# Optimization experiments

Measured on AMD Instinct MI355X. Metric: run time of the kernel, lower is better.

The kernel has to match this reference:

```python
import jax, jax.numpy as jnp
import numpy as np

B, L, D_MODEL = 2, 1024, 512
N_LAYERS = 4
D_INNER = 2 * D_MODEL          # expand=2
D_STATE = 16
D_CONV = 4
DT_RANK = D_MODEL // 16        # ceil(512/16)=32
EPS = 1e-5


def layernorm(x, w, b):
    m = jnp.mean(x, axis=-1, keepdims=True)
    v = jnp.var(x, axis=-1, keepdims=True)
    return (x - m) * jax.lax.rsqrt(v + EPS) * w + b


def selective_scan(u, delta, A, Bm, Cm, Dp):
    # u, delta: [b,l,d]; Bm, Cm: [b,l,n]; A: [d,n]; Dp: [d]
    def step(h, inp):
        dt_t, b_t, c_t, u_t = inp            # [b,d],[b,n],[b,n],[b,d]
        dA = jnp.exp(dt_t[:, :, None] * A)   # [b,d,n]
        h = dA * h + (dt_t * u_t)[:, :, None] * b_t[:, None, :]
        y = jnp.einsum('bdn,bn->bd', h, c_t)
        return h, y

    b, l, d = u.shape
    n = A.shape[1]
    h0 = jnp.zeros((b, d, n), u.dtype)
    xs = (jnp.swapaxes(delta, 0, 1), jnp.swapaxes(Bm, 0, 1),
          jnp.swapaxes(Cm, 0, 1), jnp.swapaxes(u, 0, 1))
    _, ys = jax.lax.scan(step, h0, xs)       # ys: [l,b,d]
    return jnp.swapaxes(ys, 0, 1) + u * Dp


def mamba(x, in_w, conv_w, conv_b, xp_w, dtp_w, dtp_b, A_log, Dp, out_w):
    # x: [b,l,D_MODEL]
    xz = x @ in_w.T                          # [b,l,2*d_inner]
    xc, z = jnp.split(xz, 2, axis=-1)
    xc = jnp.swapaxes(xc, 1, 2)              # [b,d_inner,l]
    xc = jax.lax.conv_general_dilated(
        xc, conv_w[:, None, :], (1,), [(D_CONV - 1, 0)],
        feature_group_count=D_INNER,
        dimension_numbers=('NCH', 'OIH', 'NCH')) + conv_b[None, :, None]
    xc = jax.nn.silu(jnp.swapaxes(xc, 1, 2))  # [b,l,d_inner]
    x_dbl = xc @ xp_w.T                       # [b,l,dt_rank+2n]
    dt = x_dbl[..., :DT_RANK]
    Bm = x_dbl[..., DT_RANK:DT_RANK + D_STATE]
    Cm = x_dbl[..., DT_RANK + D_STATE:]
    dt = jax.nn.softplus(dt @ dtp_w.T + dtp_b)
    A = -jnp.exp(A_log)
    y = selective_scan(xc, dt, A, Bm, Cm, Dp)
    y = y * jax.nn.silu(z)
    return y @ out_w.T


def forward(x, in_proj_w, conv_w, conv_b, x_proj_w, dt_proj_w, dt_proj_b,
            A_log, D_param, out_proj_w, ln_w, ln_b, fnorm_w, fnorm_b):
    residual = None
    for i in range(in_proj_w.shape[0]):
        residual = x if residual is None else x + residual
        xn = layernorm(x, ln_w[i], ln_b[i])  # norm of incoming x (as in torch src)
        h1 = mamba(xn, in_proj_w[i, 0], conv_w[i, 0], conv_b[i, 0],
                   x_proj_w[i, 0], dt_proj_w[i, 0], dt_proj_b[i, 0],
                   A_log[i, 0], D_param[i, 0], out_proj_w[i, 0])
        h2 = mamba(jnp.flip(xn, axis=1), in_proj_w[i, 1], conv_w[i, 1],
                   conv_b[i, 1], x_proj_w[i, 1], dt_proj_w[i, 1],
                   dt_proj_b[i, 1], A_log[i, 1], D_param[i, 1],
                   out_proj_w[i, 1])
        x = h1 + h2                           # bi_add: NOT flipped back, faithful
    x = x + residual
    return layernorm(x, fnorm_w, fnorm_b)


def setup_inputs() -> dict:
    key = jax.random.key(0)
    ks = jax.random.split(key, 8)
    P2 = (N_LAYERS, 2)
    inp = {}
    inp['x'] = jax.random.normal(ks[0], (B, L, D_MODEL), jnp.float32)
    inp['in_proj_w'] = jax.random.normal(ks[1], P2 + (2 * D_INNER, D_MODEL), jnp.float32) * 0.02
    inp['conv_w'] = jax.random.normal(ks[2], P2 + (D_INNER, D_CONV), jnp.float32) * 0.1
    inp['conv_b'] = jnp.zeros(P2 + (D_INNER,), jnp.float32)
    inp['x_proj_w'] = jax.random.normal(ks[3], P2 + (DT_RANK + 2 * D_STATE, D_INNER), jnp.float32) * 0.02
    inp['dt_proj_w'] = jax.random.normal(ks[4], P2 + (D_INNER, DT_RANK), jnp.float32) * (DT_RANK ** -0.5)
    inp['dt_proj_b'] = jnp.full(P2 + (D_INNER,), float(np.log(np.expm1(0.01))), jnp.float32)
    inp['A_log'] = jnp.broadcast_to(jnp.log(jnp.arange(1, D_STATE + 1, dtype=jnp.float32)), P2 + (D_INNER, D_STATE)).copy()
    inp['D_param'] = jnp.ones(P2 + (D_INNER,), jnp.float32)
    inp['out_proj_w'] = jax.random.normal(ks[5], P2 + (D_MODEL, D_INNER), jnp.float32) * 0.02
    inp['ln_w'] = jnp.ones((N_LAYERS, D_MODEL), jnp.float32)
    inp['ln_b'] = jnp.zeros((N_LAYERS, D_MODEL), jnp.float32)
    inp['fnorm_w'] = jnp.ones((D_MODEL,), jnp.float32)
    inp['fnorm_b'] = jnp.zeros((D_MODEL,), jnp.float32)
    return inp


def reference(x, in_proj_w, conv_w, conv_b, x_proj_w, dt_proj_w, dt_proj_b,
              A_log, D_param, out_proj_w, ln_w, ln_b, fnorm_w, fnorm_b):
    return forward(x, in_proj_w, conv_w, conv_b, x_proj_w, dt_proj_w,
                   dt_proj_b, A_log, D_param, out_proj_w, ln_w, ln_b,
                   fnorm_w, fnorm_b)
```

## Files before the change

kernel.cpp:

```cpp
#include <hip/hip_runtime.h>
#include <hip/hip_bf16.h>
#include <type_traits>

#define B_   2
#define L_   1024
#define DM   512
#define DI   1024
#define DS   16
#define DTR  32
#define ROWS (B_*L_)
#define NCH  32
#define CHUNK (L_/NCH)

#define PO_CW    0
#define PO_CB    32768
#define PO_XPW   40960
#define PO_DTW   565248
#define PO_DTB   827392
#define PO_ALOG  835584
#define PO_DP    966656
#define PO_LNW   974848
#define PO_LNB   976896
#define PO_FNW   978944
#define PO_FNB   979456
#define PO_END   979968

#define N_WIN    (4*2097152)
#define N_WOUT   (4*1048576)
#define N_X      1048576

typedef __bf16 bf16x8 __attribute__((ext_vector_type(8)));
typedef float  f32x4  __attribute__((ext_vector_type(4)));
using bf16 = __hip_bfloat16;

__device__ __forceinline__ bf16x8 ld8(const bf16* p){
    return *reinterpret_cast<const bf16x8*>(p);
}
__device__ __forceinline__ float b2f(bf16 v){ return __bfloat162float(v); }

__device__ __forceinline__ unsigned pkbf2(float a, float b){
    bf16 ha = __float2bfloat16(a), hb = __float2bfloat16(b);
    unsigned short ua = *(unsigned short*)&ha, ub = *(unsigned short*)&hb;
    return (unsigned)ua | ((unsigned)ub << 16);
}
__device__ __forceinline__ float unpk_lo(unsigned v){
    unsigned x = v << 16; return __builtin_bit_cast(float, x);
}
__device__ __forceinline__ float unpk_hi(unsigned v){
    unsigned x = v & 0xffff0000u; return __builtin_bit_cast(float, x);
}

__device__ __forceinline__ void async_cp16(const void* g, void* s){
    __builtin_amdgcn_global_load_lds(
        (const __attribute__((address_space(1))) unsigned int*)g,
        (__attribute__((address_space(3))) unsigned int*)s, 16, 0, 0);
}

__global__ void detect_kernel(const void* Dp_raw, int* flag){
    *flag = (*(const unsigned int*)Dp_raw == 0x3F800000u) ? 1 : 0;
}

__device__ __forceinline__ bf16 cvload(const void* s, long o, int f){
    return f ? __float2bfloat16(((const float*)s)[o]) : ((const bf16*)s)[o];
}

__global__ void megacvt_kernel(const void* cw, const void* cb, const void* xpw,
                               const void* dtw, const void* dtb, const void* al,
                               const void* dp, const void* lnw, const void* lnb,
                               const void* fnw, const void* fnb,
                               const void* inw, const void* outw, const void* xin,
                               bf16* PP, bf16* WIN, bf16* WOUT,
                               float* X, float* R, const int* flag){
    long i = (long)blockIdx.x*256 + threadIdx.x;
    int f = *flag;
    if (i < PO_END){
        const void* s; long o;
        if      (i < PO_CB)   { s = cw;  o = i; }
        else if (i < PO_XPW)  { s = cb;  o = i - PO_CB; }
        else if (i < PO_DTW)  { s = xpw; o = i - PO_XPW; }
        else if (i < PO_DTB)  { s = dtw; o = i - PO_DTW; }
        else if (i < PO_ALOG) { s = dtb; o = i - PO_DTB; }
        else if (i < PO_DP)   { s = al;  o = i - PO_ALOG; }
        else if (i < PO_LNW)  { s = dp;  o = i - PO_DP; }
        else if (i < PO_LNB)  { s = lnw; o = i - PO_LNW; }
        else if (i < PO_FNW)  { s = lnb; o = i - PO_LNB; }
        else if (i < PO_FNB)  { s = fnw; o = i - PO_FNW; }
        else                  { s = fnb; o = i - PO_FNB; }
        PP[i] = cvload(s, o, f);
        return;
    }
    i -= PO_END;
    if (i < N_WIN){ WIN[i] = cvload(inw, i, f); return; }
    i -= N_WIN;
    if (i < N_WOUT){
        long l = i >> 20, r = i & 1048575;
        long n = r >> 11, dir = (r >> 10) & 1, d = r & 1023;
        WOUT[i] = cvload(outw, ((l*2 + dir)*512 + n)*1024 + d, f);
        return;
    }
    i -= N_WOUT;
    if (i < N_X){
        X[i] = f ? ((const float*)xin)[i] : b2f(((const bf16*)xin)[i]);
        R[i] = 0.f;
    }
}

__global__ void ln_kernel(const float* __restrict__ P, int nparts,
                          float* __restrict__ R,
                          const bf16* __restrict__ w, const bf16* __restrict__ b,
                          void* __restrict__ out, int mode, const int* flag){
    int row = blockIdx.x, lane = threadIdx.x;
    size_t base = (size_t)row*DM + lane*8;
    float v[8];
    *(float4*)&v[0] = *(const float4*)(P+base);
    *(float4*)&v[4] = *(const float4*)(P+base+4);
    for (int k=1; k<nparts; ++k){
        float4 a0 = *(const float4*)(P + (size_t)k*1048576 + base);
        float4 a1 = *(const float4*)(P + (size_t)k*1048576 + base + 4);
        v[0]+=a0.x; v[1]+=a0.y; v[2]+=a0.z; v[3]+=a0.w;
        v[4]+=a1.x; v[5]+=a1.y; v[6]+=a1.z; v[7]+=a1.w;
    }
    if (mode == 0){
        float4 r0 = *(const float4*)(R+base);
        float4 r1 = *(const float4*)(R+base+4);
        r0.x += v[0]; r0.y += v[1]; r0.z += v[2]; r0.w += v[3];
        r1.x += v[4]; r1.y += v[5]; r1.z += v[6]; r1.w += v[7];
        *(float4*)(R+base)   = r0;
        *(float4*)(R+base+4) = r1;
    } else {
        float4 r0 = *(const float4*)(R+base);
        float4 r1 = *(const float4*)(R+base+4);
        v[0]+=r0.x; v[1]+=r0.y; v[2]+=r0.z; v[3]+=r0.w;
        v[4]+=r1.x; v[5]+=r1.y; v[6]+=r1.z; v[7]+=r1.w;
    }
    float s=0.f, sq=0.f;
    #pragma unroll
    for (int j=0;j<8;++j){ s += v[j]; sq += v[j]*v[j]; }
    #pragma unroll
    for (int off=32; off>=1; off>>=1){
        s  += __shfl_xor(s,  off, 64);
        sq += __shfl_xor(sq, off, 64);
    }
    float mean = s*(1.f/DM);
    float var  = sq*(1.f/DM) - mean*mean;
    float rs   = rsqrtf(var + 1e-5f);
    bf16x8 wv = ld8(w + lane*8), bv = ld8(b + lane*8);
    float res[8];
    #pragma unroll
    for (int j=0;j<8;++j)
        res[j] = (v[j]-mean)*rs*(float)wv[j] + (float)bv[j];
    if (mode == 1 && *flag){
        float* of = (float*)out;
        *(float4*)(of+base)   = make_float4(res[0],res[1],res[2],res[3]);
        *(float4*)(of+base+4) = make_float4(res[4],res[5],res[6],res[7]);
    } else {
        union { bf16 h[8]; uint4 u; } o;
        #pragma unroll
        for (int j=0;j<8;++j) o.h[j] = __float2bfloat16(res[j]);
        *(uint4*)((bf16*)out + base) = o.u;
    }
}

template<int WM, int WN, int SK, int BK, typename CT>
__global__ __launch_bounds__(WM*WN*64)
void gemm_lds(const bf16* __restrict__ A, const bf16* __restrict__ W,
              CT* __restrict__ C, int K, int lda, int ldw, int ldc,
              int selTiles, long wSel){
    constexpr int BM = WM*64, BN = WN*64, T = WM*WN*64;
    constexpr int KC = BK/8;
    constexpr int RA = (BM*KC)/T, RB = (BN*KC)/T;
    __shared__ __align__(16) bf16 sA[BM*BK];
    __shared__ __align__(16) bf16 sB[BN*BK];
    int tid = threadIdx.x;
    int mtile = blockIdx.y, ntile = blockIdx.x;
    if (mtile >= selTiles) W += wSel;
    int m0 = mtile*BM, n0 = ntile*BN;
    int kPer = K/SK, kBeg = blockIdx.z*kPer, kEnd = kBeg + kPer;
    if (SK > 1)
        C += (size_t)blockIdx.z * (size_t)(gridDim.y*BM) * (size_t)(gridDim.x*BN);
    int wave = tid>>6, lane = tid&63, quad = lane>>4, r = lane&15;
    int wrow = wave / WN, wcol = wave % WN;
    const bf16* Abase = A + (size_t)m0*lda;
    const bf16* Wbase = W + (size_t)n0*ldw;
    f32x4 acc[4][4] = {};
    for (int k0 = kBeg; k0 < kEnd; k0 += BK){
        #pragma unroll
        for (int rr=0; rr<RA; ++rr){
            int q = rr*T + tid;
            int row = q/KC, cp = q%KC;
            async_cp16(Abase + (size_t)row*lda + k0 + cp*8, &sA[q*8]);
        }
        #pragma unroll
        for (int rr=0; rr<RB; ++rr){
            int q = rr*T + tid;
            int row = q/KC, cp = q%KC;
            async_cp16(Wbase + (size_t)row*ldw + k0 + cp*8, &sB[q*8]);
        }
        __syncthreads();
        #pragma unroll
        for (int ko=0; ko<BK; ko+=32){
            bf16x8 af[4], bw[4];
            #pragma unroll
            for (int mt=0; mt<4; ++mt)
                af[mt] = *(const bf16x8*)&sA[(wrow*64 + mt*16 + r)*BK + ko + quad*8];
            #pragma unroll
            for (int nt=0; nt<4; ++nt)
                bw[nt] = *(const bf16x8*)&sB[(wcol*64 + nt*16 + r)*BK + ko + quad*8];
            #pragma unroll
            for (int mt=0; mt<4; ++mt)
                #pragma unroll
                for (int nt=0; nt<4; ++nt)
                    acc[mt][nt] = __builtin_amdgcn_mfma_f32_16x16x32_bf16(
                        af[mt], bw[nt], acc[mt][nt], 0,0,0);
        }
        __syncthreads();
    }
    #pragma unroll
    for (int mt=0; mt<4; ++mt){
        #pragma unroll
        for (int nt=0; nt<4; ++nt){
            int col = n0 + wcol*64 + nt*16 + r;
            #pragma unroll
            for (int ri=0; ri<4; ++ri){
                int row = m0 + wrow*64 + mt*16 + quad*4 + ri;
                size_t idx = (size_t)row*ldc + col;
                if constexpr (std::is_same<CT, bf16>::value)
                    C[idx] = __float2bfloat16(acc[mt][nt][ri]);
                else
                    C[idx] = acc[mt][nt][ri];
            }
        }
    }
}

__global__ void conv_kernel(const bf16* __restrict__ XZ, const bf16* __restrict__ cw,
                            const bf16* __restrict__ cb, const bf16* __restrict__ Dp,
                            bf16* __restrict__ XC, unsigned* __restrict__ GU){
    int id  = blockIdx.x*256 + threadIdx.x;
    int d   = (id & 511) * 2;
    int t   = (id >> 9) & (L_-1);
    int b   = (id >> 19) & 1;
    int dir = id >> 20;
    bf16x8 wv8 = ld8(cw + ((size_t)dir*DI + d)*4);
    unsigned pcb = *(const unsigned*)&cb[dir*DI + d];
    float acc0 = unpk_lo(pcb), acc1 = unpk_hi(pcb);
    #pragma unroll
    for (int k=0;k<4;++k){
        int tau = t - 3 + k;
        if (tau >= 0){
            int sig = dir ? (L_-1-tau) : tau;
            unsigned pz = *(const unsigned*)&XZ[((size_t)(b*L_ + sig))*4096 + dir*2048 + d];
            acc0 += (float)wv8[k]   * unpk_lo(pz);
            acc1 += (float)wv8[4+k] * unpk_hi(pz);
        }
    }
    float u0 = acc0 * (1.f/(1.f + __expf(-acc0)));
    float u1 = acc1 * (1.f/(1.f + __expf(-acc1)));
    size_t idx = ((size_t)dir*ROWS + (size_t)b*L_ + t)*DI + d;
    *(unsigned*)&XC[idx] = pkbf2(u0, u1);
    int sig3 = dir ? (L_-1-t) : t;
    unsigned pzz = *(const unsigned*)&XZ[((size_t)(b*L_ + sig3))*4096 + dir*2048 + 1024 + d];
    float z0 = unpk_lo(pzz), z1 = unpk_hi(pzz);
    float g0 = z0*(1.f/(1.f + __expf(-z0)));
    float g1 = z1*(1.f/(1.f + __expf(-z1)));
    unsigned pdv = *(const unsigned*)&Dp[dir*DI + d];
    *(uint2*)&GU[idx] = make_uint2(pkbf2(g0, u0*unpk_lo(pdv)*g0),
                                   pkbf2(g1, u1*unpk_hi(pdv)*g1));
}

__global__ void dtproj_kernel(const float* __restrict__ PX, const bf16* __restrict__ dtw,
                              const bf16* __restrict__ dtb, const bf16* __restrict__ XC,
                              unsigned* __restrict__ DTW, float* __restrict__ XD){
    int id  = blockIdx.x*256 + threadIdx.x;
    int d   = id & (DI-1);
    int row = (id >> 10) & (ROWS-1);
    int dir = id >> 21;
    int tid = threadIdx.x;
    int grow = dir*2048 + row;
    __shared__ float sXR[32];
    if (tid < 32){
        float s = 0.f;
        #pragma unroll
        for (int k=0;k<8;++k) s += PX[(size_t)k*262144 + (size_t)grow*64 + tid];
        sXR[tid] = s;
    } else if (tid < 64 && ((id >> 8) & 3) == 0){
        int j = tid - 32;
        float s = 0.f;
        #pragma unroll
        for (int k=0;k<8;++k) s += PX[(size_t)k*262144 + (size_t)grow*64 + 32 + j];
        XD[(size_t)row*128 + dir*64 + 32 + j] = s;
    }
    __syncthreads();
    const bf16* wp = dtw + ((size_t)dir*DI + d)*DTR;
    float acc = b2f(dtb[dir*DI + d]);
    #pragma unroll
    for (int kk=0;kk<4;++kk){
        bf16x8 wv = ld8(wp + kk*8);
        #pragma unroll
        for (int j=0;j<8;++j) acc += sXR[kk*8+j]*(float)wv[j];
    }
    float sp = acc > 20.f ? acc : log1pf(__expf(acc));
    size_t idx = ((size_t)dir*ROWS + row)*DI + d;
    float u = b2f(XC[idx]);
    DTW[idx] = pkbf2(sp, sp*u);
}

template<int PHASE>
__global__ __launch_bounds__(256)
void scan_phase(const unsigned* __restrict__ DTW, const unsigned* __restrict__ GU,
                const float* __restrict__ XD, const bf16* __restrict__ Al,
                float* __restrict__ SP, float* __restrict__ SH,
                bf16* __restrict__ Y){
    int dirb = blockIdx.z, dir = dirb >> 1, b = dirb & 1;
    int c    = blockIdx.y;
    int d0   = blockIdx.x*128;
    int tid  = threadIdx.x;
    int dl   = tid >> 1, nh = tid & 1;
    int d    = d0 + dl;

    __shared__ __align__(16) unsigned sDTW[CHUNK*128];
    __shared__ __align__(16) float    sBC[CHUNK][32];
    __shared__ __align__(16) unsigned sGU[(PHASE==3)?CHUNK*128:4];

    const unsigned* DTWb = DTW + ((size_t)dir*ROWS + b*L_ + c*CHUNK)*DI + d0;
    #pragma unroll
    for (int it=0; it<4; ++it){
        int q = it*256 + tid;
        int t = q >> 5, c4 = q & 31;
        async_cp16(DTWb + (size_t)t*DI + c4*4, &sDTW[q*4]);
    }
    if (PHASE == 3){
        const unsigned* GUb = GU + ((size_t)dir*ROWS + b*L_ + c*CHUNK)*DI + d0;
        #pragma unroll
        for (int it=0; it<4; ++it){
            int q = it*256 + tid;
            int t = q >> 5, c4 = q & 31;
            async_cp16(GUb + (size_t)t*DI + c4*4, &sGU[q*4]);
        }
    }
    {
        int t = tid >> 3, j = tid & 7;
        async_cp16(XD + ((size_t)(b*L_) + c*CHUNK + t)*128 + dir*64 + 32 + j*4,
                   &sBC[t][j*4]);
    }

    float An[8];
    {
        const bf16* ap = Al + ((size_t)dir*DI + d)*DS + nh*8;
        bf16x8 av = ld8(ap);
        #pragma unroll
        for (int j=0;j<8;++j) An[j] = -__expf((float)av[j]);
    }

    float h[8], pr[8];
    #pragma unroll
    for (int j=0;j<8;++j){ h[j]=0.f; pr[j]=1.f; }
    size_t so = ((size_t)(dirb*NCH + c)*DI + d)*DS + nh*8;
    if (PHASE == 3){
        for (int cc=0; cc<c; ++cc){
            size_t o = ((size_t)(dirb*NCH + cc)*DI + d)*DS + nh*8;
            f32x4 p0 = *(const f32x4*)&SP[o];
            f32x4 p1 = *(const f32x4*)&SP[o+4];
            f32x4 h0 = *(const f32x4*)&SH[o];
            f32x4 h1 = *(const f32x4*)&SH[o+4];
            #pragma unroll
            for (int j=0;j<4;++j){
                h[j]   = p0[j]*h[j]   + h0[j];
                h[4+j] = p1[j]*h[4+j] + h1[j];
            }
        }
    }
    __syncthreads();

    bf16* Yp = Y + ((size_t)b*L_ + c*CHUNK)*2048 + dir*DI + d;

    #pragma unroll 4
    for (int tl=0; tl<CHUNK; ++tl){
        unsigned dw = sDTW[tl*128 + dl];
        float dtv = unpk_lo(dw), wv = unpk_hi(dw);
        f32x4 Bv0 = *(const f32x4*)&sBC[tl][nh*8];
        f32x4 Bv1 = *(const f32x4*)&sBC[tl][nh*8+4];
        f32x4 Cv0 = *(const f32x4*)&sBC[tl][16+nh*8];
        f32x4 Cv1 = *(const f32x4*)&sBC[tl][16+nh*8+4];
        float y = 0.f;
        #pragma unroll
        for (int j=0;j<4;++j){
            float dA0 = __expf(dtv*An[j]);
            float dA1 = __expf(dtv*An[4+j]);
            h[j]   = dA0*h[j]   + wv*Bv0[j];
            h[4+j] = dA1*h[4+j] + wv*Bv1[j];
            if (PHASE == 1){ pr[j] *= dA0; pr[4+j] *= dA1; }
            else { y += h[j]*Cv0[j]; y += h[4+j]*Cv1[j]; }
        }
        if (PHASE == 3){
            y += __shfl_xor(y, 1, 64);
            if (nh == 0){
                unsigned gu = sGU[tl*128 + dl];
                Yp[(size_t)tl*2048] = __float2bfloat16(y*unpk_lo(gu) + unpk_hi(gu));
            }
        }
    }
    if (PHASE == 1){
        *(f32x4*)&SP[so]   = *(f32x4*)&pr[0];
        *(f32x4*)&SP[so+4] = *(f32x4*)&pr[4];
        *(f32x4*)&SH[so]   = *(f32x4*)&h[0];
        *(f32x4*)&SH[so+4] = *(f32x4*)&h[4];
    }
}

extern "C" void kernel_launch(void* const* d_in, const int* in_sizes, int n_in,
                              void* d_out, int out_size, void* d_ws, size_t ws_size,
                              hipStream_t stream){
    const void* x_raw    = d_in[0];
    const void* inw_raw  = d_in[1];
    const void* convw_raw= d_in[2];
    const void* convb_raw= d_in[3];
    const void* xpw_raw  = d_in[4];
    const void* dtw_raw  = d_in[5];
    const void* dtb_raw  = d_in[6];
    const void* alog_raw = d_in[7];
    const void* dp_raw   = d_in[8];
    const void* outw_raw = d_in[9];
    const void* lnw_raw  = d_in[10];
    const void* lnb_raw  = d_in[11];
    const void* fnw_raw  = d_in[12];
    const void* fnb_raw  = d_in[13];

    char* ws = (char*)d_ws;
    float*    X   = (float*)   (ws + 0);
    float*    R   = (float*)   (ws + 4194304);
    bf16*     XN  = (bf16*)    (ws + 8388608);
    bf16*     XZ  = (bf16*)    (ws + 10485760);
    bf16*     XC  = (bf16*)    (ws + 27262976);
    float*    XD  = (float*)   (ws + 35651584);
    unsigned* DTW = (unsigned*)(ws + 36700160);
    unsigned* GU  = (unsigned*)(ws + 52428800);
    bf16*     Y   = (bf16*)    (ws + 68157440);
    float*    SP  = (float*)   (ws + 76546048);
    float*    SH  = (float*)   (ws + 84934656);
    bf16*     PP  = (bf16*)    (ws + 93323264);
    bf16*     WIN = (bf16*)    (ws + 95420416);
    bf16*     WOUT= (bf16*)    (ws + 112197632);
    float*    PX  = (float*)   (ws + 120586240);
    float*    PO  = (float*)   (ws + 128974848);
    int*      FLAG= (int*)     (ws + 145752064);

    detect_kernel<<<1,1,0,stream>>>(dp_raw, FLAG);
    {
        long total = (long)PO_END + N_WIN + N_WOUT + N_X;
        int blocks = (int)((total + 255)/256);
        megacvt_kernel<<<blocks,256,0,stream>>>(
            convw_raw, convb_raw, xpw_raw, dtw_raw, dtb_raw, alog_raw, dp_raw,
            lnw_raw, lnb_raw, fnw_raw, fnb_raw, inw_raw, outw_raw, x_raw,
            PP, WIN, WOUT, X, R, FLAG);
    }

    for (int l=0; l<4; ++l){
        ln_kernel<<<ROWS,64,0,stream>>>(l==0 ? X : PO, l==0 ? 1 : 4, R,
                                        PP+PO_LNW+l*DM, PP+PO_LNB+l*DM, XN, 0, FLAG);

        gemm_lds<2,2,1,64,bf16><<<dim3(32,16,1),256,0,stream>>>(
            XN, WIN + (size_t)l*2097152, XZ, 512, 512, 512, 4096, 1<<30, 0);

        conv_kernel<<<8192,256,0,stream>>>(XZ, PP+PO_CW + (size_t)l*2*DI*4,
                                           PP+PO_CB + l*2*DI, PP+PO_DP + l*2*DI,
                                           XC, GU);

        gemm_lds<2,1,8,64,float><<<dim3(1,32,8),128,0,stream>>>(
            XC, PP+PO_XPW + (size_t)l*2*64*DI, PX, 1024, 1024, 1024, 64,
            16, (long)64*DI);

        dtproj_kernel<<<16384,256,0,stream>>>(PX, PP+PO_DTW + (size_t)l*2*DI*DTR,
                                              PP+PO_DTB + l*2*DI, XC, DTW, XD);

        scan_phase<1><<<dim3(DI/128,NCH,4),256,0,stream>>>(
            DTW, GU, XD, PP+PO_ALOG + (size_t)l*2*DI*DS, SP, SH, Y);
        scan_phase<3><<<dim3(DI/128,NCH,4),256,0,stream>>>(
            DTW, GU, XD, PP+PO_ALOG + (size_t)l*2*DI*DS, SP, SH, Y);

        gemm_lds<2,2,4,64,float><<<dim3(4,16,4),256,0,stream>>>(
            Y, WOUT + (size_t)l*1048576, PO, 2048, 2048, 2048, 512, 1<<30, 0);
    }

    ln_kernel<<<ROWS,64,0,stream>>>(PO, 4, R, PP+PO_FNW, PP+PO_FNB, d_out, 1, FLAG);
}
```

Measured before the change: 705.6 us.

## Add chunk-prefix scan kernel and vectorize weight conversion kernel

```diff
diff --git a/kernel.cpp b/kernel.cpp
--- a/kernel.cpp
+++ b/kernel.cpp
@@ -60,8 +60,20 @@
     *flag = (*(const unsigned int*)Dp_raw == 0x3F800000u) ? 1 : 0;
 }
 
-__device__ __forceinline__ bf16 cvload(const void* s, long o, int f){
-    return f ? __float2bfloat16(((const float*)s)[o]) : ((const bf16*)s)[o];
+__device__ __forceinline__ uint4 cv8(const void* s, long o, int f){
+    union { bf16 h[8]; uint4 u; } v;
+    if (f){
+        const float* p = (const float*)s + o;
+        float4 a = *(const float4*)p;
+        float4 b = *(const float4*)(p+4);
+        v.h[0]=__float2bfloat16(a.x); v.h[1]=__float2bfloat16(a.y);
+        v.h[2]=__float2bfloat16(a.z); v.h[3]=__float2bfloat16(a.w);
+        v.h[4]=__float2bfloat16(b.x); v.h[5]=__float2bfloat16(b.y);
+        v.h[6]=__float2bfloat16(b.z); v.h[7]=__float2bfloat16(b.w);
+    } else {
+        v.u = *(const uint4*)((const bf16*)s + o);
+    }
+    return v.u;
 }
 
 __global__ void megacvt_kernel(const void* cw, const void* cb, const void* xpw,
@@ -71,7 +83,7 @@
                                const void* inw, const void* outw, const void* xin,
                                bf16* PP, bf16* WIN, bf16* WOUT,
                                float* X, float* R, const int* flag){
-    long i = (long)blockIdx.x*256 + threadIdx.x;
+    long i = ((long)blockIdx.x*256 + threadIdx.x) * 8;
     int f = *flag;
     if (i < PO_END){
         const void* s; long o;
@@ -86,22 +98,35 @@
         else if (i < PO_FNW)  { s = lnb; o = i - PO_LNB; }
         else if (i < PO_FNB)  { s = fnw; o = i - PO_FNW; }
         else                  { s = fnb; o = i - PO_FNB; }
-        PP[i] = cvload(s, o, f);
+        *(uint4*)&PP[i] = cv8(s, o, f);
         return;
     }
     i -= PO_END;
-    if (i < N_WIN){ WIN[i] = cvload(inw, i, f); return; }
+    if (i < N_WIN){ *(uint4*)&WIN[i] = cv8(inw, i, f); return; }
     i -= N_WIN;
     if (i < N_WOUT){
         long l = i >> 20, r = i & 1048575;
         long n = r >> 11, dir = (r >> 10) & 1, d = r & 1023;
-        WOUT[i] = cvload(outw, ((l*2 + dir)*512 + n)*1024 + d, f);
+        *(uint4*)&WOUT[i] = cv8(outw, ((l*2 + dir)*512 + n)*1024 + d, f);
         return;
     }
     i -= N_WOUT;
     if (i < N_X){
-        X[i] = f ? ((const float*)xin)[i] : b2f(((const bf16*)xin)[i]);
-        R[i] = 0.f;
+        float xv[8];
+        if (f){
+            *(float4*)&xv[0] = *(const float4*)((const float*)xin + i);
+            *(float4*)&xv[4] = *(const float4*)((const float*)xin + i + 4);
+        } else {
+            union { uint4 u; bf16 h[8]; } w;
+            w.u = *(const uint4*)((const bf16*)xin + i);
+            #pragma unroll
+            for (int j=0;j<8;++j) xv[j] = b2f(w.h[j]);
+        }
+        *(float4*)(X+i)   = make_float4(xv[0],xv[1],xv[2],xv[3]);
+        *(float4*)(X+i+4) = make_float4(xv[4],xv[5],xv[6],xv[7]);
+        float4 z = make_float4(0.f,0.f,0.f,0.f);
+        *(float4*)(R+i)   = z;
+        *(float4*)(R+i+4) = z;
     }
 }
 
@@ -305,12 +330,26 @@
     DTW[idx] = pkbf2(sp, sp*u);
 }
 
+__global__ void scan_mid(const float* __restrict__ SP, const float* __restrict__ SH,
+                         float* __restrict__ H0){
+    int id   = blockIdx.x*256 + threadIdx.x;
+    int dirb = id >> 14;
+    int rest = id & 16383;
+    float h = 0.f;
+    #pragma unroll
+    for (int c=0; c<NCH; ++c){
+        size_t o = ((size_t)(dirb*NCH + c) << 14) + rest;
+        H0[o] = h;
+        h = SP[o]*h + SH[o];
+    }
+}
+
 template<int PHASE>
 __global__ __launch_bounds__(256)
 void scan_phase(const unsigned* __restrict__ DTW, const unsigned* __restrict__ GU,
                 const float* __restrict__ XD, const bf16* __restrict__ Al,
                 float* __restrict__ SP, float* __restrict__ SH,
-                bf16* __restrict__ Y){
+                const float* __restrict__ H0, bf16* __restrict__ Y){
     int dirb = blockIdx.z, dir = dirb >> 1, b = dirb & 1;
     int c    = blockIdx.y;
     int d0   = blockIdx.x*128;
@@ -353,23 +392,18 @@
     }
 
     float h[8], pr[8];
-    #pragma unroll
-    for (int j=0;j<8;++j){ h[j]=0.f; pr[j]=1.f; }
     size_t so = ((size_t)(dirb*NCH + c)*DI + d)*DS + nh*8;
     if (PHASE == 3){
-        for (int cc=0; cc<c; ++cc){
-            size_t o = ((size_t)(dirb*NCH + cc)*DI + d)*DS + nh*8;
-            f32x4 p0 = *(const f32x4*)&SP[o];
-            f32x4 p1 = *(const f32x4*)&SP[o+4];
-            f32x4 h0 = *(const f32x4*)&SH[o];
-            f32x4 h1 = *(const f32x4*)&SH[o+4];
-            #pragma unroll
-            for (int j=0;j<4;++j){
-                h[j]   = p0[j]*h[j]   + h0[j];
-                h[4+j] = p1[j]*h[4+j] + h1[j];
-            }
-        }
-    }
+        f32x4 h0a = *(const f32x4*)&H0[so];
+        f32x4 h0b = *(const f32x4*)&H0[so+4];
+        #pragma unroll
+        for (int j=0;j<4;++j){ h[j] = h0a[j]; h[4+j] = h0b[j]; }
+    } else {
+        #pragma unroll
+        for (int j=0;j<8;++j) h[j] = 0.f;
+    }
+    #pragma unroll
+    for (int j=0;j<8;++j) pr[j] = 1.f;
     __syncthreads();
 
     bf16* Yp = Y + ((size_t)b*L_ + c*CHUNK)*2048 + dir*DI + d;
@@ -444,10 +478,11 @@
     float*    PX  = (float*)   (ws + 120586240);
     float*    PO  = (float*)   (ws + 128974848);
     int*      FLAG= (int*)     (ws + 145752064);
+    float*    H0  = (float*)   (ws + 145752128);
 
     detect_kernel<<<1,1,0,stream>>>(dp_raw, FLAG);
     {
-        long total = (long)PO_END + N_WIN + N_WOUT + N_X;
+        long total = ((long)PO_END + N_WIN + N_WOUT + N_X) / 8;
         int blocks = (int)((total + 255)/256);
         megacvt_kernel<<<blocks,256,0,stream>>>(
             convw_raw, convb_raw, xpw_raw, dtw_raw, dtb_raw, alog_raw, dp_raw,
@@ -474,9 +509,10 @@
                                               PP+PO_DTB + l*2*DI, XC, DTW, XD);
 
         scan_phase<1><<<dim3(DI/128,NCH,4),256,0,stream>>>(
-            DTW, GU, XD, PP+PO_ALOG + (size_t)l*2*DI*DS, SP, SH, Y);
+            DTW, GU, XD, PP+PO_ALOG + (size_t)l*2*DI*DS, SP, SH, H0, Y);
+        scan_mid<<<256,256,0,stream>>>(SP, SH, H0);
         scan_phase<3><<<dim3(DI/128,NCH,4),256,0,stream>>>(
-            DTW, GU, XD, PP+PO_ALOG + (size_t)l*2*DI*DS, SP, SH, Y);
+            DTW, GU, XD, PP+PO_ALOG + (size_t)l*2*DI*DS, SP, SH, H0, Y);
 
         gemm_lds<2,2,4,64,float><<<dim3(4,16,4),256,0,stream>>>(
             Y, WOUT + (size_t)l*1048576, PO, 2048, 2048, 2048, 512, 1<<30, 0);
```

Result: faster. 666.3 us (-5.6%).
